# Kernel optimization log

Measured on AMD Instinct MI355X. Metric: run time of the kernel, lower is better.

## Reference

```python
import jax, jax.numpy as jnp
import numpy as np

B, C, H, W = 2, 512, 128, 128
L_NUM, HEADS, LEVELS, POINTS = 6, 8, 1, 4
HEAD_DIM = C // HEADS


def setup_inputs() -> dict:
    key = jax.random.key(0)
    ks = jax.random.split(key, 16)
    s = 0.02
    rn = lambda k, shape, scale=s: jax.random.normal(k, shape, jnp.float32) * scale
    return dict(
        bev_feat=jax.random.normal(ks[0], (B, C, H, W), jnp.float32),
        lidar_feat=jax.random.normal(ks[1], (B, C, H, W), jnp.float32),
        Wv=rn(ks[2], (L_NUM, C, C)), bv=jnp.zeros((L_NUM, C), jnp.float32),
        Woff=rn(ks[3], (L_NUM, C, HEADS * LEVELS * POINTS * 2)),
        boff=rn(ks[4], (L_NUM, HEADS * LEVELS * POINTS * 2), 0.5),
        Waw=rn(ks[5], (L_NUM, C, HEADS * LEVELS * POINTS)),
        baw=jnp.zeros((L_NUM, HEADS * LEVELS * POINTS), jnp.float32),
        Wout=rn(ks[6], (L_NUM, C, C)), bout=jnp.zeros((L_NUM, C), jnp.float32),
        ln1_g=jnp.ones((L_NUM, C), jnp.float32), ln1_b=jnp.zeros((L_NUM, C), jnp.float32),
        W1=rn(ks[7], (L_NUM, C, C)), W2=rn(ks[8], (L_NUM, C, C)),
        ln2_g=jnp.ones((L_NUM, C), jnp.float32), ln2_b=jnp.zeros((L_NUM, C), jnp.float32),
        pe_W1=rn(ks[9], (2, C), 0.5),
        pe_bn_g=jnp.ones((C,), jnp.float32), pe_bn_b=jnp.zeros((C,), jnp.float32),
        pe_bn_m=jnp.zeros((C,), jnp.float32), pe_bn_v=jnp.ones((C,), jnp.float32),
        pe_W2=rn(ks[10], (C, C)),
    )


def _layer_norm(x, g, b):
    mu = jnp.mean(x, -1, keepdims=True)
    var = jnp.mean((x - mu) ** 2, -1, keepdims=True)
    return (x - mu) * jax.lax.rsqrt(var + 1e-5) * g + b


def _bilinear_gather(v_flat, locx, locy):
    # v_flat: (B, heads, H*W, d); locx/locy: (B, heads, S) normalized [0,1]
    # grid_sample semantics: align_corners=False, zero padding
    x = locx * W - 0.5
    y = locy * H - 0.5
    x0f = jnp.floor(x); y0f = jnp.floor(y)
    wx = x - x0f; wy = y - y0f
    x0 = x0f.astype(jnp.int32); y0 = y0f.astype(jnp.int32)

    def corner(xi, yi, w):
        inb = (xi >= 0) & (xi < W) & (yi >= 0) & (yi < H)
        idx = jnp.clip(yi, 0, H - 1) * W + jnp.clip(xi, 0, W - 1)
        g = jnp.take_along_axis(v_flat, idx[..., None], axis=2)
        return g * (w * inb)[..., None]

    return (corner(x0, y0, (1 - wx) * (1 - wy)) + corner(x0 + 1, y0, wx * (1 - wy))
            + corner(x0, y0 + 1, (1 - wx) * wy) + corner(x0 + 1, y0 + 1, wx * wy))


def reference(bev_feat, lidar_feat, Wv, bv, Woff, boff, Waw, baw, Wout, bout,
              ln1_g, ln1_b, W1, W2, ln2_g, ln2_b,
              pe_W1, pe_bn_g, pe_bn_b, pe_bn_m, pe_bn_v, pe_W2):
    N = H * W
    # sparse voxelization: keep rows with all-nonzero features, pack valid-first per batch
    lf = jnp.transpose(lidar_feat, (0, 2, 3, 1)).reshape(B, N, C)
    mask = jnp.all(lf != 0, axis=-1)                       # (B,N)
    order = jnp.argsort((~mask).astype(jnp.int32), axis=1, stable=True)  # valid first
    valid = jnp.take_along_axis(mask, order, axis=1)       # (B,N)
    q = jnp.take_along_axis(lf, order[..., None], axis=1) * valid[..., None]
    hh = jnp.arange(N) // W
    ww = jnp.arange(N) % W
    ref_all = jnp.stack([ww / W, hh / H], -1).astype(jnp.float32)  # (N,2) = (x,y)
    ref = jnp.broadcast_to(ref_all, (B, N, 2))
    ref = jnp.take_along_axis(ref, order[..., None], axis=1) * valid[..., None]
    # learned positional embedding (BatchNorm in eval mode)
    pe = ref.reshape(B * N, 2) @ pe_W1
    pe = (pe - pe_bn_m) * jax.lax.rsqrt(pe_bn_v + 1e-5) * pe_bn_g + pe_bn_b
    q_pos = (jax.nn.relu(pe) @ pe_W2).reshape(B, N, C)
    feat_flat = jnp.transpose(bev_feat.reshape(B, C, N), (0, 2, 1))  # (B,N,C)
    norm_xy = jnp.array([W, H], jnp.float32)  # offset normalizer per level (w,h)
    for i in range(L_NUM):
        ident = q
        x = q + q_pos
        v = (feat_flat @ Wv[i] + bv[i]).reshape(B, N, HEADS, HEAD_DIM)
        v_flat = jnp.transpose(v, (0, 2, 1, 3))  # (B,heads,N,d)
        off = (x @ Woff[i] + boff[i]).reshape(B, N, HEADS, LEVELS * POINTS, 2)
        aw = jax.nn.softmax((x @ Waw[i] + baw[i]).reshape(B, N, HEADS, LEVELS * POINTS), axis=-1)
        loc = ref[:, :, None, None, :] + off / norm_xy      # (B,N,heads,P,2)
        locx = jnp.transpose(loc[..., 0], (0, 2, 1, 3)).reshape(B, HEADS, N * POINTS)
        locy = jnp.transpose(loc[..., 1], (0, 2, 1, 3)).reshape(B, HEADS, N * POINTS)
        samp = _bilinear_gather(v_flat, locx, locy).reshape(B, HEADS, N, POINTS, HEAD_DIM)
        awt = jnp.transpose(aw, (0, 2, 1, 3))               # (B,heads,N,P)
        out = jnp.sum(samp * awt[..., None], axis=3)        # (B,heads,N,d)
        out = jnp.transpose(out, (0, 2, 1, 3)).reshape(B, N, C)
        q = out @ Wout[i] + bout[i] + ident                 # dropout in eval = identity
        q = _layer_norm(q, ln1_g[i], ln1_b[i])
        q = jax.nn.relu(q @ W1[i]) @ W2[i] + q
        q = _layer_norm(q, ln2_g[i], ln2_b[i])
    # scatter back to dense (B,C,H,W); invalid voxels stay zero
    slots = jnp.zeros((B, N, C), q.dtype)
    slots = slots.at[jnp.arange(B)[:, None], order].set(q * valid[..., None])
    return jnp.transpose(slots.reshape(B, H, W, C), (0, 3, 1, 2))
```

## Files before the change

### kernel.cpp

```cpp
#include <hip/hip_runtime.h>
#include <cstdint>
#include <cstddef>

#define BDIM 2
#define CDIM 512
#define HDIM 128
#define WDIM 128
#define NDIM (HDIM * WDIM)
#define LNUM 6
#define NHEADS 8
#define HEAD_DIM 64
#define NPTS 4
#define BN_TOT (BDIM * NDIM)

typedef unsigned short u16;
typedef __attribute__((ext_vector_type(8))) short bf16x8;
typedef __attribute__((ext_vector_type(4))) float f32x4;

__device__ __forceinline__ u16 f2bf(float x) {
    unsigned u = __float_as_uint(x);
    u += 0x7fffu + ((u >> 16) & 1u);
    return (u16)(u >> 16);
}
__device__ __forceinline__ float bf2f(u16 h) {
    return __uint_as_float(((unsigned)h) << 16);
}

__device__ __forceinline__ void load_lds16(const void* g, void* l) {
    __builtin_amdgcn_global_load_lds(
        (const __attribute__((address_space(1))) void*)g,
        (__attribute__((address_space(3))) void*)l, 16, 0, 0);
}

__device__ __forceinline__ void wait_vm16() { asm volatile("s_waitcnt vmcnt(16)" ::: "memory"); }
__device__ __forceinline__ void wait_vm12() { asm volatile("s_waitcnt vmcnt(12)" ::: "memory"); }
__device__ __forceinline__ void wait_vm8()  { asm volatile("s_waitcnt vmcnt(8)" ::: "memory"); }
__device__ __forceinline__ void wait_vm4()  { asm volatile("s_waitcnt vmcnt(4)" ::: "memory"); }
__device__ __forceinline__ void wait_vm0()  { asm volatile("s_waitcnt vmcnt(0)" ::: "memory"); }
__device__ __forceinline__ void sbar()  { __builtin_amdgcn_s_barrier(); }
__device__ __forceinline__ void spin()  { __builtin_amdgcn_sched_barrier(0); }

__global__ void mask_kernel(const float* __restrict__ lidar, int* __restrict__ mask)
{
    int idx = blockIdx.x * blockDim.x + threadIdx.x;
    if (idx >= BN_TOT) return;
    int b = idx / NDIM;
    int n = idx - b * NDIM;
    const float* p = lidar + (size_t)b * CDIM * NDIM + n;
    int ok = 1;
#pragma unroll 8
    for (int c = 0; c < CDIM; ++c)
        ok &= (p[(size_t)c * NDIM] != 0.0f);
    mask[idx] = ok;
}

__global__ void order_kernel(const int* __restrict__ mask, int* __restrict__ order,
                             int* __restrict__ nvalid)
{
    int b = blockIdx.x;
    const int* m = mask + b * NDIM;
    int* ord = order + b * NDIM;
    __shared__ int part[256];
    __shared__ int totalValid;
    int t = threadIdx.x;
    const int CHUNK = NDIM / 256;
    int base = t * CHUNK;
    int cnt = 0;
    for (int i = 0; i < CHUNK; ++i) cnt += m[base + i];
    part[t] = cnt;
    __syncthreads();
    for (int s = 1; s < 256; s <<= 1) {
        int v = (t >= s) ? part[t - s] : 0;
        __syncthreads();
        part[t] += v;
        __syncthreads();
    }
    if (t == 255) { totalValid = part[255]; nvalid[b] = part[255]; }
    __syncthreads();
    int validBefore = (t == 0) ? 0 : part[t - 1];
    int nv = totalValid;
    for (int i = 0; i < CHUNK; ++i) {
        int n = base + i;
        if (m[n]) { ord[validBefore] = n; validBefore++; }
        else      { int invBefore = n - validBefore; ord[nv + invBefore] = n; }
    }
}

__global__ void ref_kernel(const int* __restrict__ order, const int* __restrict__ nvalid,
                           float* __restrict__ ref)
{
    int idx = blockIdx.x * blockDim.x + threadIdx.x;
    if (idx >= BN_TOT) return;
    int b = idx / NDIM;
    int j = idx - b * NDIM;
    int n = order[idx];
    float flag = (j < nvalid[b]) ? 1.0f : 0.0f;
    int hh = n / WDIM;
    int ww = n - hh * WDIM;
    ref[(size_t)idx * 2 + 0] = ((float)ww / (float)WDIM) * flag;
    ref[(size_t)idx * 2 + 1] = ((float)hh / (float)HDIM) * flag;
}

__global__ void pack_q_kernel(const float* __restrict__ lidar, const int* __restrict__ order,
                              const int* __restrict__ nvalid, u16* __restrict__ q)
{
    __shared__ float tile[32][33];
    __shared__ int ord_s[32];
    int b  = blockIdx.z;
    int j0 = blockIdx.x * 32;
    int c0 = blockIdx.y * 32;
    int tx = threadIdx.x, ty = threadIdx.y;
    if (ty == 0) ord_s[tx] = order[b * NDIM + j0 + tx];
    __syncthreads();
    const float* src = lidar + (size_t)b * CDIM * NDIM;
#pragma unroll
    for (int k = 0; k < 4; ++k) {
        int cl = ty * 4 + k;
        tile[cl][tx] = src[(size_t)(c0 + cl) * NDIM + ord_s[tx]];
    }
    __syncthreads();
    int nv = nvalid[b];
#pragma unroll
    for (int k = 0; k < 4; ++k) {
        int jl = ty * 4 + k;
        int j = j0 + jl;
        float f = (j < nv) ? 1.0f : 0.0f;
        q[((size_t)b * NDIM + j) * CDIM + c0 + tx] = f2bf(tile[tx][jl] * f);
    }
}

__global__ void scatter_kernel(const u16* __restrict__ q, const int* __restrict__ order,
                               const int* __restrict__ nvalid, float* __restrict__ out)
{
    __shared__ float tile[32][33];
    __shared__ int ord_s[32];
    int b  = blockIdx.z;
    int j0 = blockIdx.x * 32;
    int c0 = blockIdx.y * 32;
    int tx = threadIdx.x, ty = threadIdx.y;
    if (ty == 0) ord_s[tx] = order[b * NDIM + j0 + tx];
    __syncthreads();
    int nv = nvalid[b];
#pragma unroll
    for (int k = 0; k < 4; ++k) {
        int jl = ty * 4 + k;
        int j = j0 + jl;
        float f = (j < nv) ? 1.0f : 0.0f;
        tile[jl][tx] = bf2f(q[((size_t)b * NDIM + j) * CDIM + c0 + tx]) * f;
    }
    __syncthreads();
    float* dst = out + (size_t)b * CDIM * NDIM;
#pragma unroll
    for (int k = 0; k < 4; ++k) {
        int cl = ty * 4 + k;
        dst[(size_t)(c0 + cl) * NDIM + ord_s[tx]] = tile[tx][cl];
    }
}

__global__ void tconv_b_kernel(const float* __restrict__ src0, u16* __restrict__ dst0)
{
    __shared__ float t[32][33];
    int z = blockIdx.z;
    const float* src = src0 + (size_t)z * 512 * 512;
    u16* dst = dst0 + (size_t)z * 512 * 512;
    int k0 = blockIdx.x * 32, n0 = blockIdx.y * 32;
    int tx = threadIdx.x, ty = threadIdx.y;
#pragma unroll
    for (int j = 0; j < 4; ++j) {
        int kl = ty * 4 + j;
        t[kl][tx] = src[(size_t)(k0 + kl) * 512 + n0 + tx];
    }
    __syncthreads();
#pragma unroll
    for (int j = 0; j < 4; ++j) {
        int nl = ty * 4 + j;
        dst[(size_t)(n0 + nl) * 512 + k0 + tx] = f2bf(t[tx][nl]);
    }
}

__global__ void tconv_offaw_b_kernel(const float* __restrict__ woff0,
                                     const float* __restrict__ waw0,
                                     u16* __restrict__ dst0)
{
    __shared__ float t[32][33];
    int z = blockIdx.z;
    const float* woff = woff0 + (size_t)z * 512 * 64;
    const float* waw  = waw0 + (size_t)z * 512 * 32;
    u16* dst = dst0 + (size_t)z * 96 * 512;
    int k0 = blockIdx.x * 32, n0 = blockIdx.y * 32;
    int tx = threadIdx.x, ty = threadIdx.y;
#pragma unroll
    for (int j = 0; j < 4; ++j) {
        int kl = ty * 4 + j;
        int n = n0 + tx;
        float v = (n < 64) ? woff[(size_t)(k0 + kl) * 64 + n]
                           : waw[(size_t)(k0 + kl) * 32 + (n - 64)];
        t[kl][tx] = v;
    }
    __syncthreads();
#pragma unroll
    for (int j = 0; j < 4; ++j) {
        int nl = ty * 4 + j;
        dst[(size_t)(n0 + nl) * 512 + k0 + tx] = f2bf(t[tx][nl]);
    }
}

__global__ void bev_conv_kernel(const float* __restrict__ bev, u16* __restrict__ dst)
{
    __shared__ float t[32][33];
    int b  = blockIdx.z;
    int n0 = blockIdx.x * 32;
    int c0 = blockIdx.y * 32;
    int tx = threadIdx.x, ty = threadIdx.y;
    const float* src = bev + (size_t)b * CDIM * NDIM;
#pragma unroll
    for (int j = 0; j < 4; ++j) {
        int cl = ty * 4 + j;
        t[cl][tx] = src[(size_t)(c0 + cl) * NDIM + n0 + tx];
    }
    __syncthreads();
#pragma unroll
    for (int j = 0; j < 4; ++j) {
        int nl = ty * 4 + j;
        dst[((size_t)b * NDIM + n0 + nl) * CDIM + c0 + tx] = f2bf(t[tx][nl]);
    }
}

__global__ void pe_hidden_kernel(const float* __restrict__ ref, const float* __restrict__ W1,
                                 const float* __restrict__ g, const float* __restrict__ bb,
                                 const float* __restrict__ m, const float* __restrict__ v,
                                 u16* __restrict__ out)
{
    int row = blockIdx.x;
    float r0 = ref[(size_t)row * 2 + 0];
    float r1 = ref[(size_t)row * 2 + 1];
    for (int c = threadIdx.x; c < CDIM; c += blockDim.x) {
        float pe = r0 * W1[c] + r1 * W1[CDIM + c];
        pe = (pe - m[c]) * rsqrtf(v[c] + 1e-5f) * g[c] + bb[c];
        out[(size_t)row * CDIM + c] = f2bf(fmaxf(pe, 0.0f));
    }
}

__global__ void add_bf_kernel(const u16* __restrict__ q, const u16* __restrict__ qpos,
                              u16* __restrict__ x)
{
    size_t i = (size_t)blockIdx.x * blockDim.x + threadIdx.x;
    uint4 qa = ((const uint4*)q)[i];
    uint4 pv = ((const uint4*)qpos)[i];
    unsigned qw[4] = {qa.x, qa.y, qa.z, qa.w};
    unsigned pw[4] = {pv.x, pv.y, pv.z, pv.w};
    unsigned rw[4];
#pragma unroll
    for (int k = 0; k < 4; ++k) {
        float a0 = bf2f((u16)(qw[k] & 0xffff)), a1 = bf2f((u16)(qw[k] >> 16));
        float p0 = bf2f((u16)(pw[k] & 0xffff)), p1 = bf2f((u16)(pw[k] >> 16));
        rw[k] = (unsigned)f2bf(a0 + p0) | ((unsigned)f2bf(a1 + p1) << 16);
    }
    uint4 r; r.x = rw[0]; r.y = rw[1]; r.z = rw[2]; r.w = rw[3];
    ((uint4*)x)[i] = r;
}

__global__ __launch_bounds__(512) void gemm_bf16(
    const u16* __restrict__ A, const u16* __restrict__ Bt,
    const float* __restrict__ bias, u16* __restrict__ outB, int relu)
{
    __shared__ u16 As[4][256 * 32];
    __shared__ u16 Bs[4][256 * 32];
    int tid = threadIdx.x;
    int wave = tid >> 6, lane = tid & 63;
    int wr = wave >> 2, wc = wave & 3;
    int quad = lane >> 4, l15 = lane & 15;
    int lid = blockIdx.x;
    int tsw = (lid & 7) * 32 + (lid >> 3);
    int bm = (tsw >> 1) * 256, bn = (tsw & 1) * 256;

    f32x4 acc[8][4];
#pragma unroll
    for (int i = 0; i < 8; ++i)
#pragma unroll
        for (int j = 0; j < 4; ++j) { f32x4 z = {0.f, 0.f, 0.f, 0.f}; acc[i][j] = z; }

    int c0 = wave * 2, c1 = wave * 2 + 1;
    const u16* Ag0 = A  + (size_t)(bm + c0 * 16 + (lane >> 2)) * 512 + (lane & 3) * 8;
    const u16* Ag1 = A  + (size_t)(bm + c1 * 16 + (lane >> 2)) * 512 + (lane & 3) * 8;
    const u16* Bg0 = Bt + (size_t)(bn + c0 * 16 + (lane >> 2)) * 512 + (lane & 3) * 8;
    const u16* Bg1 = Bt + (size_t)(bn + c1 * 16 + (lane >> 2)) * 512 + (lane & 3) * 8;

#pragma unroll
    for (int k = 0; k < 3; ++k) {
        load_lds16(Ag0 + k * 32, &As[k][c0 * 512]);
        load_lds16(Ag1 + k * 32, &As[k][c1 * 512]);
        load_lds16(Bg0 + k * 32, &Bs[k][c0 * 512]);
        load_lds16(Bg1 + k * 32, &Bs[k][c1 * 512]);
    }

    for (int it = 0; it < 16; ++it) {
        sbar();  spin();
        int cur = it & 3;
        if (it < 13) {
            int nb = (it + 3) & 3;
            int kn = (it + 3) * 32;
            load_lds16(Ag0 + kn, &As[nb][c0 * 512]);
            load_lds16(Ag1 + kn, &As[nb][c1 * 512]);
            load_lds16(Bg0 + kn, &Bs[nb][c0 * 512]);
            load_lds16(Bg1 + kn, &Bs[nb][c1 * 512]);
            wait_vm12();
        } else if (it == 13) {
            wait_vm8();
        } else if (it == 14) {
            wait_vm4();
        } else {
            wait_vm0();
        }
        sbar();  spin();
        bf16x8 av[8], bv[4];
#pragma unroll
        for (int mi = 0; mi < 8; ++mi)
            av[mi] = *(const bf16x8*)&As[cur][(wr * 128 + mi * 16 + l15) * 32 + quad * 8];
#pragma unroll
        for (int ni = 0; ni < 4; ++ni)
            bv[ni] = *(const bf16x8*)&Bs[cur][(wc * 64 + ni * 16 + l15) * 32 + quad * 8];
#pragma unroll
        for (int mi = 0; mi < 8; ++mi)
#pragma unroll
            for (int ni = 0; ni < 4; ++ni)
                acc[mi][ni] = __builtin_amdgcn_mfma_f32_16x16x32_bf16(
                    av[mi], bv[ni], acc[mi][ni], 0, 0, 0);
    }

    int rowb = bm + wr * 128;
    int colb = bn + wc * 64;
#pragma unroll
    for (int mi = 0; mi < 8; ++mi) {
#pragma unroll
        for (int ni = 0; ni < 4; ++ni) {
            int col = colb + ni * 16 + l15;
            float bi = bias ? bias[col] : 0.0f;
#pragma unroll
            for (int r = 0; r < 4; ++r) {
                int row = rowb + mi * 16 + quad * 4 + r;
                float val = acc[mi][ni][r] + bi;
                if (relu) val = fmaxf(val, 0.0f);
                outB[(size_t)row * 512 + col] = f2bf(val);
            }
        }
    }
}

__global__ __launch_bounds__(256) void gemm_residf(
    const u16* __restrict__ A, const u16* __restrict__ Bt,
    const float* __restrict__ bias, const u16* __restrict__ resid,
    float* __restrict__ outY)
{
    __shared__ u16 As[3][128 * 32];
    __shared__ u16 Bs[3][128 * 32];
    int tid = threadIdx.x;
    int wave = tid >> 6, lane = tid & 63;
    int wr = wave >> 1, wc = wave & 1;
    int quad = lane >> 4, l15 = lane & 15;
    int lid = blockIdx.x;
    int tsw = (lid & 7) * 64 + (lid >> 3);
    int bm = (tsw >> 2) * 128, bn = (tsw & 3) * 128;

    f32x4 acc[4][4];
#pragma unroll
    for (int i = 0; i < 4; ++i)
#pragma unroll
        for (int j = 0; j < 4; ++j) { f32x4 z = {0.f, 0.f, 0.f, 0.f}; acc[i][j] = z; }

    int ch0 = wave, ch1 = wave + 4;
    const u16* Ag0 = A  + (size_t)(bm + ch0 * 16 + (lane >> 2)) * 512 + (lane & 3) * 8;
    const u16* Ag1 = A  + (size_t)(bm + ch1 * 16 + (lane >> 2)) * 512 + (lane & 3) * 8;
    const u16* Bg0 = Bt + (size_t)(bn + ch0 * 16 + (lane >> 2)) * 512 + (lane & 3) * 8;
    const u16* Bg1 = Bt + (size_t)(bn + ch1 * 16 + (lane >> 2)) * 512 + (lane & 3) * 8;

#pragma unroll
    for (int k = 0; k < 2; ++k) {
        load_lds16(Ag0 + k * 32, &As[k][ch0 * 512]);
        load_lds16(Ag1 + k * 32, &As[k][ch1 * 512]);
        load_lds16(Bg0 + k * 32, &Bs[k][ch0 * 512]);
        load_lds16(Bg1 + k * 32, &Bs[k][ch1 * 512]);
    }

    for (int it = 0; it < 16; ++it) {
        sbar();  spin();
        int cur = it % 3;
        if (it < 14) {
            int nb = (it + 2) % 3;
            int kn = (it + 2) * 32;
            load_lds16(Ag0 + kn, &As[nb][ch0 * 512]);
            load_lds16(Ag1 + kn, &As[nb][ch1 * 512]);
            load_lds16(Bg0 + kn, &Bs[nb][ch0 * 512]);
            load_lds16(Bg1 + kn, &Bs[nb][ch1 * 512]);
            wait_vm8();
        } else if (it == 14) {
            wait_vm4();
        } else {
            wait_vm0();
        }
        sbar();  spin();
        bf16x8 av[4], bv[4];
#pragma unroll
        for (int mi = 0; mi < 4; ++mi)
            av[mi] = *(const bf16x8*)&As[cur][(wr * 64 + mi * 16 + l15) * 32 + quad * 8];
#pragma unroll
        for (int ni = 0; ni < 4; ++ni)
            bv[ni] = *(const bf16x8*)&Bs[cur][(wc * 64 + ni * 16 + l15) * 32 + quad * 8];
#pragma unroll
        for (int mi = 0; mi < 4; ++mi)
#pragma unroll
            for (int ni = 0; ni < 4; ++ni)
                acc[mi][ni] = __builtin_amdgcn_mfma_f32_16x16x32_bf16(
                    av[mi], bv[ni], acc[mi][ni], 0, 0, 0);
    }

    int rowb = bm + wr * 64;
    int colb = bn + wc * 64;
#pragma unroll
    for (int mi = 0; mi < 4; ++mi) {
#pragma unroll
        for (int ni = 0; ni < 4; ++ni) {
            int col = colb + ni * 16 + l15;
            float bi = bias ? bias[col] : 0.0f;
#pragma unroll
            for (int r = 0; r < 4; ++r) {
                int row = rowb + mi * 16 + quad * 4 + r;
                size_t off = (size_t)row * 512 + col;
                outY[off] = acc[mi][ni][r] + bi + bf2f(resid[off]);
            }
        }
    }
}

__global__ __launch_bounds__(256) void ln_f(
    const float* __restrict__ Y, const float* __restrict__ g,
    const float* __restrict__ bta, u16* __restrict__ outQ)
{
    int row  = blockIdx.x * 4 + (threadIdx.x >> 6);
    int lane = threadIdx.x & 63;
    size_t base = (size_t)row * CDIM + lane * 8;

    float4 y0 = *(const float4*)(Y + base);
    float4 y1 = *(const float4*)(Y + base + 4);
    float v[8] = {y0.x, y0.y, y0.z, y0.w, y1.x, y1.y, y1.z, y1.w};

    float s = 0.f, s2 = 0.f;
#pragma unroll
    for (int j = 0; j < 8; ++j) { s += v[j]; s2 += v[j] * v[j]; }
#pragma unroll
    for (int m = 1; m < 64; m <<= 1) {
        s  += __shfl_xor(s, m, 64);
        s2 += __shfl_xor(s2, m, 64);
    }
    float mu = s * (1.0f / 512.0f);
    float var = s2 * (1.0f / 512.0f) - mu * mu;
    float iv = rsqrtf(var + 1e-5f);

    int c0 = lane * 8;
    float4 g0 = *(const float4*)(g + c0);
    float4 g1 = *(const float4*)(g + c0 + 4);
    float4 b0 = *(const float4*)(bta + c0);
    float4 b1 = *(const float4*)(bta + c0 + 4);
    float gl[8] = {g0.x, g0.y, g0.z, g0.w, g1.x, g1.y, g1.z, g1.w};
    float bl[8] = {b0.x, b0.y, b0.z, b0.w, b1.x, b1.y, b1.z, b1.w};

    unsigned qw[4];
#pragma unroll
    for (int k = 0; k < 4; ++k) {
        float a = (v[2 * k]     - mu) * iv * gl[2 * k]     + bl[2 * k];
        float b = (v[2 * k + 1] - mu) * iv * gl[2 * k + 1] + bl[2 * k + 1];
        qw[k] = (unsigned)f2bf(a) | ((unsigned)f2bf(b) << 16);
    }
    uint4 qo; qo.x = qw[0]; qo.y = qw[1]; qo.z = qw[2]; qo.w = qw[3];
    *(uint4*)(outQ + base) = qo;
}

__global__ __launch_bounds__(256) void gemm_offaw(
    const u16* __restrict__ A, const u16* __restrict__ Bt,
    const float* __restrict__ boff, const float* __restrict__ baw,
    u16* __restrict__ offb, u16* __restrict__ awb)
{
    __shared__ u16 As[3][128 * 32];
    __shared__ u16 Bs[3][128 * 32];
    int tid = threadIdx.x;
    int wave = tid >> 6, lane = tid & 63;
    int wr = wave >> 1, wc = wave & 1;
    int quad = lane >> 4, l15 = lane & 15;
    int bm = blockIdx.y * 128;

    f32x4 acc[4][4];
#pragma unroll
    for (int i = 0; i < 4; ++i)
#pragma unroll
        for (int j = 0; j < 4; ++j) { f32x4 z = {0.f, 0.f, 0.f, 0.f}; acc[i][j] = z; }

    const u16* Ag[4];
    const u16* Bg[4];
#pragma unroll
    for (int s = 0; s < 4; ++s) {
        Ag[s] = A + (size_t)(bm + wr * 64 + s * 16 + (lane >> 2)) * 512 + (lane & 3) * 8;
        int br = wc * 64 + s * 16 + (lane >> 2);
        if (br > 95) br = 95;
        Bg[s] = Bt + (size_t)br * 512 + (lane & 3) * 8;
    }

#pragma unroll
    for (int k = 0; k < 2; ++k)
#pragma unroll
        for (int s = 0; s < 4; ++s) {
            load_lds16(Ag[s] + k * 32, &As[k][(wr * 4 + s) * 512]);
            load_lds16(Bg[s] + k * 32, &Bs[k][(wc * 4 + s) * 512]);
        }

    for (int it = 0; it < 16; ++it) {
        sbar();
        int cur = it % 3;
        if (it < 14) {
            int nb = (it + 2) % 3;
            int kn = (it + 2) * 32;
#pragma unroll
            for (int s = 0; s < 4; ++s) {
                load_lds16(Ag[s] + kn, &As[nb][(wr * 4 + s) * 512]);
                load_lds16(Bg[s] + kn, &Bs[nb][(wc * 4 + s) * 512]);
            }
            wait_vm16();
        } else if (it == 14) {
            wait_vm8();
        } else {
            wait_vm0();
        }
        bf16x8 av[4], bv[4];
#pragma unroll
        for (int mi = 0; mi < 4; ++mi)
            av[mi] = *(const bf16x8*)&As[cur][(wr * 64 + mi * 16 + l15) * 32 + quad * 8];
#pragma unroll
        for (int ni = 0; ni < 4; ++ni)
            bv[ni] = *(const bf16x8*)&Bs[cur][(wc * 64 + ni * 16 + l15) * 32 + quad * 8];
#pragma unroll
        for (int mi = 0; mi < 4; ++mi)
#pragma unroll
            for (int ni = 0; ni < 4; ++ni)
                acc[mi][ni] = __builtin_amdgcn_mfma_f32_16x16x32_bf16(
                    av[mi], bv[ni], acc[mi][ni], 0, 0, 0);
    }

    int rowb = bm + wr * 64;
#pragma unroll
    for (int mi = 0; mi < 4; ++mi) {
#pragma unroll
        for (int ni = 0; ni < 4; ++ni) {
            int col = wc * 64 + ni * 16 + l15;
            if (col < 96) {
                float bi = (col < 64) ? boff[col] : baw[col - 64];
#pragma unroll
                for (int r = 0; r < 4; ++r) {
                    int row = rowb + mi * 16 + quad * 4 + r;
                    float val = acc[mi][ni][r] + bi;
                    if (col < 64) offb[(size_t)row * 64 + col] = f2bf(val);
                    else          awb[(size_t)row * 32 + (col - 64)] = f2bf(val);
                }
            }
        }
    }
}

__global__ __launch_bounds__(256) void sample_kernel(
    const float* __restrict__ ref, const u16* __restrict__ off,
    const u16* __restrict__ aw, const u16* __restrict__ v,
    u16* __restrict__ out)
{
    int bj = blockIdx.x * 4 + (threadIdx.x >> 6);
    int lane = threadIdx.x & 63;
    int h  = lane >> 3;
    int d8 = (lane & 7) * 8;
    int b  = bj >> 14;

    float rx = ref[(size_t)bj * 2 + 0];
    float ry = ref[(size_t)bj * 2 + 1];
    uint4 offv = *(const uint4*)(off + (size_t)bj * 64 + h * 8);
    uint2 awv  = *(const uint2*)(aw + (size_t)bj * 32 + h * 4);

    float l0 = bf2f((u16)(awv.x & 0xffff)), l1 = bf2f((u16)(awv.x >> 16));
    float l2 = bf2f((u16)(awv.y & 0xffff)), l3 = bf2f((u16)(awv.y >> 16));
    float mx = fmaxf(fmaxf(l0, l1), fmaxf(l2, l3));
    float e[4];
    e[0] = expf(l0 - mx); e[1] = expf(l1 - mx);
    e[2] = expf(l2 - mx); e[3] = expf(l3 - mx);
    float inv_es = 1.0f / (e[0] + e[1] + e[2] + e[3]);

    const u16* vb = v + (size_t)b * NDIM * CDIM + h * HEAD_DIM + d8;
    float acc[8] = {0.f, 0.f, 0.f, 0.f, 0.f, 0.f, 0.f, 0.f};
    unsigned ow[4] = {offv.x, offv.y, offv.z, offv.w};

#pragma unroll
    for (int p = 0; p < NPTS; ++p) {
        float ox = bf2f((u16)(ow[p] & 0xffff));
        float oy = bf2f((u16)(ow[p] >> 16));
        float X = rx * (float)WDIM + ox - 0.5f;
        float Y = ry * (float)HDIM + oy - 0.5f;
        float x0f = floorf(X), y0f = floorf(Y);
        float wx = X - x0f, wy = Y - y0f;
        int x0 = (int)x0f, y0 = (int)y0f;
        float ep = e[p];
#pragma unroll
        for (int cy = 0; cy < 2; ++cy) {
            int yy = y0 + cy;
            float wyc = cy ? wy : (1.0f - wy);
            int yin = (yy >= 0) & (yy < HDIM);
            int yc = min(max(yy, 0), HDIM - 1);
#pragma unroll
            for (int cx = 0; cx < 2; ++cx) {
                int xx = x0 + cx;
                float wxc = cx ? wx : (1.0f - wx);
                int xin = (xx >= 0) & (xx < WDIM);
                int xc = min(max(xx, 0), WDIM - 1);
                float wgt = ep * wyc * wxc * (float)(yin & xin);
                uint4 vv = *(const uint4*)(vb + (size_t)(yc * WDIM + xc) * CDIM);
                acc[0] += wgt * bf2f((u16)(vv.x & 0xffff));
                acc[1] += wgt * bf2f((u16)(vv.x >> 16));
                acc[2] += wgt * bf2f((u16)(vv.y & 0xffff));
                acc[3] += wgt * bf2f((u16)(vv.y >> 16));
                acc[4] += wgt * bf2f((u16)(vv.z & 0xffff));
                acc[5] += wgt * bf2f((u16)(vv.z >> 16));
                acc[6] += wgt * bf2f((u16)(vv.w & 0xffff));
                acc[7] += wgt * bf2f((u16)(vv.w >> 16));
            }
        }
    }
    uint4 r;
    r.x = (unsigned)f2bf(acc[0] * inv_es) | ((unsigned)f2bf(acc[1] * inv_es) << 16);
    r.y = (unsigned)f2bf(acc[2] * inv_es) | ((unsigned)f2bf(acc[3] * inv_es) << 16);
    r.z = (unsigned)f2bf(acc[4] * inv_es) | ((unsigned)f2bf(acc[5] * inv_es) << 16);
    r.w = (unsigned)f2bf(acc[6] * inv_es) | ((unsigned)f2bf(acc[7] * inv_es) << 16);
    *(uint4*)(out + (size_t)bj * CDIM + h * HEAD_DIM + d8) = r;
}

extern "C" void kernel_launch(void* const* d_in, const int* in_sizes, int n_in,
                              void* d_out, int out_size, void* d_ws, size_t ws_size,
                              hipStream_t stream)
{
    const float* bev   = (const float*)d_in[0];
    const float* lidar = (const float*)d_in[1];
    const float* Wv    = (const float*)d_in[2];
    const float* bv    = (const float*)d_in[3];
    const float* Woff  = (const float*)d_in[4];
    const float* boff  = (const float*)d_in[5];
    const float* Waw   = (const float*)d_in[6];
    const float* baw   = (const float*)d_in[7];
    const float* Wout  = (const float*)d_in[8];
    const float* bout  = (const float*)d_in[9];
    const float* ln1g  = (const float*)d_in[10];
    const float* ln1b  = (const float*)d_in[11];
    const float* W1    = (const float*)d_in[12];
    const float* W2    = (const float*)d_in[13];
    const float* ln2g  = (const float*)d_in[14];
    const float* ln2b  = (const float*)d_in[15];
    const float* peW1  = (const float*)d_in[16];
    const float* peg   = (const float*)d_in[17];
    const float* peb   = (const float*)d_in[18];
    const float* pem   = (const float*)d_in[19];
    const float* pev   = (const float*)d_in[20];
    const float* pe_W2 = (const float*)d_in[21];

    const size_t NC   = (size_t)BN_TOT * CDIM;
    const size_t HALF = NC / 2;
    const size_t WSZ  = 512 * 512;

    char* base = (char*)d_ws;
    u16* q      = (u16*)base;
    u16* actA   = (u16*)(base + NC * 2);
    u16* actB   = (u16*)(base + NC * 4);
    float* actAf = (float*)actA;
    float* actBf = (float*)actB;
    u16* wt     = (u16*)(base + NC * 6);
    u16* wtv    = wt;
    u16* wtout  = wt + 6 * WSZ;
    u16* wt1    = wt + 12 * WSZ;
    u16* wt2    = wt + 18 * WSZ;
    u16* wtpe   = wt + 24 * WSZ;
    u16* offawt = wt + 25 * WSZ;
    u16* offb   = offawt + 6 * 96 * 512;
    u16* awb    = offb + (size_t)BN_TOT * 64;
    float* refb = (float*)(awb + (size_t)BN_TOT * 32);
    int* mask   = (int*)(refb + (size_t)BN_TOT * 2);
    int* order  = mask + BN_TOT;
    int* nvalid = order + BN_TOT;

    u16* qpos_bf = (u16*)d_out;
    u16* featT   = (u16*)d_out + NC;

    dim3 blk328(32, 8);
    dim3 offaw_grid(1, 256);
    int  lnf_half = (BN_TOT / 2) / 4;
    unsigned addb = (unsigned)(NC / 8 / 256);

    mask_kernel<<<BN_TOT / 256, 256, 0, stream>>>(lidar, mask);
    order_kernel<<<BDIM, 256, 0, stream>>>(mask, order, nvalid);
    ref_kernel<<<BN_TOT / 256, 256, 0, stream>>>(order, nvalid, refb);
    pack_q_kernel<<<dim3(NDIM / 32, CDIM / 32, BDIM), blk328, 0, stream>>>(lidar, order, nvalid, q);
    bev_conv_kernel<<<dim3(NDIM / 32, CDIM / 32, BDIM), blk328, 0, stream>>>(bev, featT);

    tconv_b_kernel<<<dim3(16, 16, 6), blk328, 0, stream>>>(Wv,   wtv);
    tconv_b_kernel<<<dim3(16, 16, 6), blk328, 0, stream>>>(Wout, wtout);
    tconv_b_kernel<<<dim3(16, 16, 6), blk328, 0, stream>>>(W1,   wt1);
    tconv_b_kernel<<<dim3(16, 16, 6), blk328, 0, stream>>>(W2,   wt2);
    tconv_b_kernel<<<dim3(16, 16, 1), blk328, 0, stream>>>(pe_W2, wtpe);
    tconv_offaw_b_kernel<<<dim3(16, 3, 6), blk328, 0, stream>>>(Woff, Waw, offawt);

    pe_hidden_kernel<<<BN_TOT, 128, 0, stream>>>(refb, peW1, peg, peb, pem, pev, actA);
    gemm_bf16<<<256, 512, 0, stream>>>(actA, wtpe, nullptr, qpos_bf, 0);

    add_bf_kernel<<<addb, 256, 0, stream>>>(q, qpos_bf, actB);

    for (int i = 0; i < LNUM; ++i) {
        gemm_offaw<<<offaw_grid, 256, 0, stream>>>(actB, offawt + (size_t)i * 96 * 512,
                                                   boff + i * 64, baw + i * 32, offb, awb);
        gemm_bf16<<<256, 512, 0, stream>>>(featT, wtv + (size_t)i * WSZ,
                                           bv + i * CDIM, actA, 0);
        sample_kernel<<<BN_TOT / 4, 256, 0, stream>>>(refb, offb, awb, actA, actB);
        for (int c = 0; c < 2; ++c) {
            gemm_residf<<<512, 256, 0, stream>>>(
                actB + c * HALF, wtout + (size_t)i * WSZ, bout + i * CDIM,
                q + c * HALF, actAf);
            ln_f<<<lnf_half, 256, 0, stream>>>(
                actAf, ln1g + i * CDIM, ln1b + i * CDIM, q + c * HALF);
        }
        gemm_bf16<<<256, 512, 0, stream>>>(q, wt1 + (size_t)i * WSZ, nullptr, actA, 1);
        for (int c = 0; c < 2; ++c) {
            gemm_residf<<<512, 256, 0, stream>>>(
                actA + c * HALF, wt2 + (size_t)i * WSZ, nullptr,
                q + c * HALF, actBf);
            ln_f<<<lnf_half, 256, 0, stream>>>(
                actBf, ln2g + i * CDIM, ln2b + i * CDIM, q + c * HALF);
        }
        if (i < LNUM - 1)
            add_bf_kernel<<<addb, 256, 0, stream>>>(q, qpos_bf, actB);
    }

    scatter_kernel<<<dim3(NDIM / 32, CDIM / 32, BDIM), blk328, 0, stream>>>(
        q, order, nvalid, (float*)d_out);
}
```

Measured before the change: 1.803 ms.

## Enlarge residual GEMM tiles, run full-batch when workspace allows, fuse qpos add into LN

The residual-output GEMM moves to 256x256 tiles with 512 threads and a four-stage LDS pipeline, matching the main bf16 GEMM. When the workspace holds a full fp32 buffer, the out-projection and FFN residual GEMMs and layer norms run over all rows in one launch each instead of two half launches. The second layer norm also writes q+qpos, which removes the separate add kernel. The change cuts launch count and aims for better MFMA reuse per tile, but needs more LDS and registers, and the fast path depends on workspace size.

```diff
diff --git a/kernel.cpp b/kernel.cpp
--- a/kernel.cpp
+++ b/kernel.cpp
@@ -271,7 +271,8 @@
     int wr = wave >> 2, wc = wave & 3;
     int quad = lane >> 4, l15 = lane & 15;
     int lid = blockIdx.x;
-    int tsw = (lid & 7) * 32 + (lid >> 3);
+    int cpx = gridDim.x >> 3;
+    int tsw = (lid & 7) * cpx + (lid >> 3);
     int bm = (tsw >> 1) * 256, bn = (tsw & 1) * 256;
 
     f32x4 acc[8][4];
@@ -347,51 +348,54 @@
     }
 }
 
-__global__ __launch_bounds__(256) void gemm_residf(
+__global__ __launch_bounds__(512) void gemm_residf(
     const u16* __restrict__ A, const u16* __restrict__ Bt,
     const float* __restrict__ bias, const u16* __restrict__ resid,
     float* __restrict__ outY)
 {
-    __shared__ u16 As[3][128 * 32];
-    __shared__ u16 Bs[3][128 * 32];
+    __shared__ u16 As[4][256 * 32];
+    __shared__ u16 Bs[4][256 * 32];
     int tid = threadIdx.x;
     int wave = tid >> 6, lane = tid & 63;
-    int wr = wave >> 1, wc = wave & 1;
+    int wr = wave >> 2, wc = wave & 3;
     int quad = lane >> 4, l15 = lane & 15;
     int lid = blockIdx.x;
-    int tsw = (lid & 7) * 64 + (lid >> 3);
-    int bm = (tsw >> 2) * 128, bn = (tsw & 3) * 128;
-
-    f32x4 acc[4][4];
-#pragma unroll
-    for (int i = 0; i < 4; ++i)
+    int cpx = gridDim.x >> 3;
+    int tsw = (lid & 7) * cpx + (lid >> 3);
+    int bm = (tsw >> 1) * 256, bn = (tsw & 1) * 256;
+
+    f32x4 acc[8][4];
+#pragma unroll
+    for (int i = 0; i < 8; ++i)
 #pragma unroll
         for (int j = 0; j < 4; ++j) { f32x4 z = {0.f, 0.f, 0.f, 0.f}; acc[i][j] = z; }
 
-    int ch0 = wave, ch1 = wave + 4;
-    const u16* Ag0 = A  + (size_t)(bm + ch0 * 16 + (lane >> 2)) * 512 + (lane & 3) * 8;
-    const u16* Ag1 = A  + (size_t)(bm + ch1 * 16 + (lane >> 2)) * 512 + (lane & 3) * 8;
-    const u16* Bg0 = Bt + (size_t)(bn + ch0 * 16 + (lane >> 2)) * 512 + (lane & 3) * 8;
-    const u16* Bg1 = Bt + (size_t)(bn + ch1 * 16 + (lane >> 2)) * 512 + (lane & 3) * 8;
-
-#pragma unroll
-    for (int k = 0; k < 2; ++k) {
-        load_lds16(Ag0 + k * 32, &As[k][ch0 * 512]);
-        load_lds16(Ag1 + k * 32, &As[k][ch1 * 512]);
-        load_lds16(Bg0 + k * 32, &Bs[k][ch0 * 512]);
-        load_lds16(Bg1 + k * 32, &Bs[k][ch1 * 512]);
+    int c0 = wave * 2, c1 = wave * 2 + 1;
+    const u16* Ag0 = A  + (size_t)(bm + c0 * 16 + (lane >> 2)) * 512 + (lane & 3) * 8;
+    const u16* Ag1 = A  + (size_t)(bm + c1 * 16 + (lane >> 2)) * 512 + (lane & 3) * 8;
+    const u16* Bg0 = Bt + (size_t)(bn + c0 * 16 + (lane >> 2)) * 512 + (lane & 3) * 8;
+    const u16* Bg1 = Bt + (size_t)(bn + c1 * 16 + (lane >> 2)) * 512 + (lane & 3) * 8;
+
+#pragma unroll
+    for (int k = 0; k < 3; ++k) {
+        load_lds16(Ag0 + k * 32, &As[k][c0 * 512]);
+        load_lds16(Ag1 + k * 32, &As[k][c1 * 512]);
+        load_lds16(Bg0 + k * 32, &Bs[k][c0 * 512]);
+        load_lds16(Bg1 + k * 32, &Bs[k][c1 * 512]);
     }
 
     for (int it = 0; it < 16; ++it) {
         sbar();  spin();
-        int cur = it % 3;
-        if (it < 14) {
-            int nb = (it + 2) % 3;
-            int kn = (it + 2) * 32;
-            load_lds16(Ag0 + kn, &As[nb][ch0 * 512]);
-            load_lds16(Ag1 + kn, &As[nb][ch1 * 512]);
-            load_lds16(Bg0 + kn, &Bs[nb][ch0 * 512]);
-            load_lds16(Bg1 + kn, &Bs[nb][ch1 * 512]);
+        int cur = it & 3;
+        if (it < 13) {
+            int nb = (it + 3) & 3;
+            int kn = (it + 3) * 32;
+            load_lds16(Ag0 + kn, &As[nb][c0 * 512]);
+            load_lds16(Ag1 + kn, &As[nb][c1 * 512]);
+            load_lds16(Bg0 + kn, &Bs[nb][c0 * 512]);
+            load_lds16(Bg1 + kn, &Bs[nb][c1 * 512]);
+            wait_vm12();
+        } else if (it == 13) {
             wait_vm8();
         } else if (it == 14) {
             wait_vm4();
@@ -399,25 +403,25 @@
             wait_vm0();
         }
         sbar();  spin();
-        bf16x8 av[4], bv[4];
-#pragma unroll
-        for (int mi = 0; mi < 4; ++mi)
-            av[mi] = *(const bf16x8*)&As[cur][(wr * 64 + mi * 16 + l15) * 32 + quad * 8];
+        bf16x8 av[8], bv[4];
+#pragma unroll
+        for (int mi = 0; mi < 8; ++mi)
+            av[mi] = *(const bf16x8*)&As[cur][(wr * 128 + mi * 16 + l15) * 32 + quad * 8];
 #pragma unroll
         for (int ni = 0; ni < 4; ++ni)
             bv[ni] = *(const bf16x8*)&Bs[cur][(wc * 64 + ni * 16 + l15) * 32 + quad * 8];
 #pragma unroll
-        for (int mi = 0; mi < 4; ++mi)
+        for (int mi = 0; mi < 8; ++mi)
 #pragma unroll
             for (int ni = 0; ni < 4; ++ni)
                 acc[mi][ni] = __builtin_amdgcn_mfma_f32_16x16x32_bf16(
                     av[mi], bv[ni], acc[mi][ni], 0, 0, 0);
     }
 
-    int rowb = bm + wr * 64;
+    int rowb = bm + wr * 128;
     int colb = bn + wc * 64;
 #pragma unroll
-    for (int mi = 0; mi < 4; ++mi) {
+    for (int mi = 0; mi < 8; ++mi) {
 #pragma unroll
         for (int ni = 0; ni < 4; ++ni) {
             int col = colb + ni * 16 + l15;
@@ -434,7 +438,8 @@
 
 __global__ __launch_bounds__(256) void ln_f(
     const float* __restrict__ Y, const float* __restrict__ g,
-    const float* __restrict__ bta, u16* __restrict__ outQ)
+    const float* __restrict__ bta, u16* __restrict__ outQ,
+    const u16* __restrict__ qpos, u16* __restrict__ outX)
 {
     int row  = blockIdx.x * 4 + (threadIdx.x >> 6);
     int lane = threadIdx.x & 63;
@@ -464,15 +469,32 @@
     float gl[8] = {g0.x, g0.y, g0.z, g0.w, g1.x, g1.y, g1.z, g1.w};
     float bl[8] = {b0.x, b0.y, b0.z, b0.w, b1.x, b1.y, b1.z, b1.w};
 
+    float y[8];
+#pragma unroll
+    for (int j = 0; j < 8; ++j)
+        y[j] = (v[j] - mu) * iv * gl[j] + bl[j];
+
     unsigned qw[4];
 #pragma unroll
-    for (int k = 0; k < 4; ++k) {
-        float a = (v[2 * k]     - mu) * iv * gl[2 * k]     + bl[2 * k];
-        float b = (v[2 * k + 1] - mu) * iv * gl[2 * k + 1] + bl[2 * k + 1];
-        qw[k] = (unsigned)f2bf(a) | ((unsigned)f2bf(b) << 16);
-    }
+    for (int k = 0; k < 4; ++k)
+        qw[k] = (unsigned)f2bf(y[2 * k]) | ((unsigned)f2bf(y[2 * k + 1]) << 16);
     uint4 qo; qo.x = qw[0]; qo.y = qw[1]; qo.z = qw[2]; qo.w = qw[3];
     *(uint4*)(outQ + base) = qo;
+
+    if (outX) {
+        uint4 pv = *(const uint4*)(qpos + base);
+        unsigned pw[4] = {pv.x, pv.y, pv.z, pv.w};
+        unsigned xw[4];
+#pragma unroll
+        for (int k = 0; k < 4; ++k) {
+            float p0 = bf2f((u16)(pw[k] & 0xffff));
+            float p1 = bf2f((u16)(pw[k] >> 16));
+            xw[k] = (unsigned)f2bf(y[2 * k] + p0)
+                  | ((unsigned)f2bf(y[2 * k + 1] + p1) << 16);
+        }
+        uint4 xo; xo.x = xw[0]; xo.y = xw[1]; xo.z = xw[2]; xo.w = xw[3];
+        *(uint4*)(outX + base) = xo;
+    }
 }
 
 __global__ __launch_bounds__(256) void gemm_offaw(
@@ -685,12 +707,16 @@
     int* mask   = (int*)(refb + (size_t)BN_TOT * 2);
     int* order  = mask + BN_TOT;
     int* nvalid = order + BN_TOT;
+    const size_t YF_OFF  = (size_t)128 * 1024 * 1024;
+    const size_t YF_NEED = YF_OFF + NC * sizeof(float);
+    float* yf = (ws_size >= YF_NEED) ? (float*)(base + YF_OFF) : nullptr;
 
     u16* qpos_bf = (u16*)d_out;
     u16* featT   = (u16*)d_out + NC;
 
     dim3 blk328(32, 8);
     dim3 offaw_grid(1, 256);
+    int  lnf_full = BN_TOT / 4;
     int  lnf_half = (BN_TOT / 2) / 4;
     unsigned addb = (unsigned)(NC / 8 / 256);
 
@@ -718,23 +744,39 @@
         gemm_bf16<<<256, 512, 0, stream>>>(featT, wtv + (size_t)i * WSZ,
                                            bv + i * CDIM, actA, 0);
         sample_kernel<<<BN_TOT / 4, 256, 0, stream>>>(refb, offb, awb, actA, actB);
-        for (int c = 0; c < 2; ++c) {
-            gemm_residf<<<512, 256, 0, stream>>>(
-                actB + c * HALF, wtout + (size_t)i * WSZ, bout + i * CDIM,
-                q + c * HALF, actAf);
-            ln_f<<<lnf_half, 256, 0, stream>>>(
-                actAf, ln1g + i * CDIM, ln1b + i * CDIM, q + c * HALF);
-        }
-        gemm_bf16<<<256, 512, 0, stream>>>(q, wt1 + (size_t)i * WSZ, nullptr, actA, 1);
-        for (int c = 0; c < 2; ++c) {
-            gemm_residf<<<512, 256, 0, stream>>>(
-                actA + c * HALF, wt2 + (size_t)i * WSZ, nullptr,
-                q + c * HALF, actBf);
-            ln_f<<<lnf_half, 256, 0, stream>>>(
-                actBf, ln2g + i * CDIM, ln2b + i * CDIM, q + c * HALF);
-        }
-        if (i < LNUM - 1)
-            add_bf_kernel<<<addb, 256, 0, stream>>>(q, qpos_bf, actB);
+
+        if (yf) {
+            gemm_residf<<<256, 512, 0, stream>>>(actB, wtout + (size_t)i * WSZ,
+                                                 bout + i * CDIM, q, yf);
+            ln_f<<<lnf_full, 256, 0, stream>>>(yf, ln1g + i * CDIM, ln1b + i * CDIM,
+                                               q, nullptr, nullptr);
+            gemm_bf16<<<256, 512, 0, stream>>>(q, wt1 + (size_t)i * WSZ, nullptr, actA, 1);
+            gemm_residf<<<256, 512, 0, stream>>>(actA, wt2 + (size_t)i * WSZ,
+                                                 nullptr, q, yf);
+            ln_f<<<lnf_full, 256, 0, stream>>>(yf, ln2g + i * CDIM, ln2b + i * CDIM,
+                                               q, qpos_bf,
+                                               (i < LNUM - 1) ? actB : nullptr);
+        } else {
+            for (int c = 0; c < 2; ++c) {
+                gemm_residf<<<128, 512, 0, stream>>>(
+                    actB + c * HALF, wtout + (size_t)i * WSZ, bout + i * CDIM,
+                    q + c * HALF, actAf);
+                ln_f<<<lnf_half, 256, 0, stream>>>(
+                    actAf, ln1g + i * CDIM, ln1b + i * CDIM, q + c * HALF,
+                    nullptr, nullptr);
+            }
+            gemm_bf16<<<256, 512, 0, stream>>>(q, wt1 + (size_t)i * WSZ, nullptr, actA, 1);
+            for (int c = 0; c < 2; ++c) {
+                gemm_residf<<<128, 512, 0, stream>>>(
+                    actA + c * HALF, wt2 + (size_t)i * WSZ, nullptr,
+                    q + c * HALF, actBf);
+                ln_f<<<lnf_half, 256, 0, stream>>>(
+                    actBf, ln2g + i * CDIM, ln2b + i * CDIM, q + c * HALF,
+                    nullptr, nullptr);
+            }
+            if (i < LNUM - 1)
+                add_bf_kernel<<<addb, 256, 0, stream>>>(q, qpos_bf, actB);
+        }
     }
 
     scatter_kernel<<<dim3(NDIM / 32, CDIM / 32, BDIM), blk328, 0, stream>>>(
```

After: 1.698 ms. -5.8%, faster.
